# Kernel tuning notes

Hardware: AMD Instinct MI355X
Metric: run time of the kernel (lower is better)

Reference implementation:

```python
import jax, jax.numpy as jnp
import numpy as np

B, S, D, H = 1, 1024, 4096, 32
HD = D // H
HEAVY_RATIO = 0.1
RECENT_RATIO = 0.1


def _rotary_tables(seq_len, dim):
    inv_freq = 1.0 / (10000.0 ** (jnp.arange(0, dim, 2, dtype=jnp.float32) / dim))
    t = jnp.arange(seq_len, dtype=jnp.float32)
    freqs = jnp.outer(t, inv_freq)            # [S, dim/2]
    emb = jnp.concatenate([freqs, freqs], -1)  # [S, dim]
    return jnp.cos(emb), jnp.sin(emb)


def _rotate_half(x):
    x1, x2 = jnp.split(x, 2, axis=-1)
    return jnp.concatenate([-x2, x1], axis=-1)


def setup_inputs() -> dict:
    key = jax.random.key(0)
    ks = jax.random.split(key, 5)
    hidden_states = jax.random.normal(ks[0], (B, S, D), dtype=jnp.float32)
    neg = jnp.finfo(jnp.float32).min
    i = jnp.arange(S)[:, None]
    j = jnp.arange(S)[None, :]
    attention_mask = jnp.where(j <= i, 0.0, neg).astype(jnp.float32)[None, None]  # [1,1,S,S]
    std = 0.02
    Wq = jax.random.normal(ks[1], (D, D), dtype=jnp.float32) * std
    Wk = jax.random.normal(ks[2], (D, D), dtype=jnp.float32) * std
    Wv = jax.random.normal(ks[3], (D, D), dtype=jnp.float32) * std
    Wo = jax.random.normal(ks[4], (D, D), dtype=jnp.float32) * std
    return {"hidden_states": hidden_states, "attention_mask": attention_mask,
            "Wq": Wq, "Wk": Wk, "Wv": Wv, "Wo": Wo}


def _heavy_hitter_mask(attn_weights, heavy_budget):
    # attn_weights: [B,H,S,S] (already includes additive causal mask)
    b, h, s, _ = attn_weights.shape
    probs = jax.nn.softmax(attn_weights.astype(jnp.float32), axis=-1)  # [B,H,S,S]
    cols = jnp.arange(s)
    # accumulated score from the first heavy_budget rows; zero cols >= heavy_budget
    acc0 = probs[:, :, :heavy_budget, :].sum(axis=2) * (cols < heavy_budget)

    def scatter_true(idx):  # idx [k] -> [S] bool
        return jnp.zeros((s,), dtype=bool).at[idx].set(True)

    def step(acc, xs):
        prob_row, t = xs  # prob_row [B,H,S]
        _, topk_idx = jax.lax.top_k(acc, heavy_budget - 1)  # [B,H,k]
        m = jax.vmap(jax.vmap(scatter_true))(topk_idx)       # [B,H,S]
        m = m | (cols < 4) | (cols == t)
        acc = (acc + prob_row) * m
        return acc, m

    ts = jnp.arange(heavy_budget, s)
    rows = jnp.moveaxis(probs[:, :, heavy_budget:, :], 2, 0)  # [S-hb,B,H,S]
    _, masks = jax.lax.scan(step, acc0, (rows, ts))
    masks = jnp.moveaxis(masks, 0, 2)  # [B,H,S-hb,S]
    rows_i = jnp.arange(s)[:, None]
    init_block = (rows_i < heavy_budget) & (cols[None, :] < heavy_budget)  # [S,S]
    init_rows = jnp.broadcast_to(init_block[None, None, :heavy_budget, :], (b, h, heavy_budget, s))
    return jnp.concatenate([init_rows, masks], axis=2)  # [B,H,S,S] bool


def reference(hidden_states, attention_mask, Wq, Wk, Wv, Wo):
    bsz, q_len, d = hidden_states.shape
    hd = d // H
    # torch Linear: y = x @ W.T
    q = jnp.einsum('bsd,ed->bse', hidden_states, Wq).reshape(bsz, q_len, H, hd).transpose(0, 2, 1, 3)
    k = jnp.einsum('bsd,ed->bse', hidden_states, Wk).reshape(bsz, q_len, H, hd).transpose(0, 2, 1, 3)
    v = jnp.einsum('bsd,ed->bse', hidden_states, Wv).reshape(bsz, q_len, H, hd).transpose(0, 2, 1, 3)
    cos, sin = _rotary_tables(q_len, hd)  # [S,hd]
    cos = cos[None, None]; sin = sin[None, None]
    q = q * cos + _rotate_half(q) * sin
    k = k * cos + _rotate_half(k) * sin
    attn = jnp.einsum('bhqd,bhkd->bhqk', q, k) / jnp.sqrt(jnp.float32(hd))
    neg = jnp.finfo(attn.dtype).min
    attn = jnp.maximum(attn + attention_mask, neg)
    heavy_budget = int(HEAVY_RATIO * q_len)
    recent_budget = int(RECENT_RATIO * q_len)
    if heavy_budget > 0:
        mask_bottom = _heavy_hitter_mask(attn, heavy_budget)
    else:
        mask_bottom = jnp.zeros(attn.shape, dtype=bool)
    i = jnp.arange(q_len)[:, None]
    j = jnp.arange(q_len)[None, :]
    recent = j >= (i - recent_budget)        # triu(diagonal=-recent_budget)
    mask_bottom = (mask_bottom | recent) & (j <= i)  # then tril(diagonal=0)
    attn = jnp.where(mask_bottom, attn, jnp.min(attention_mask))
    attn = jax.nn.softmax(attn.astype(jnp.float32), axis=-1).astype(hidden_states.dtype)
    out = jnp.einsum('bhqk,bhkd->bhqd', attn, v)
    out = out.transpose(0, 2, 1, 3).reshape(bsz, q_len, d)
    return jnp.einsum('bse,de->bsd', out, Wo)
```

## Files before the change

kernel.cpp:

```cpp
#include <hip/hip_runtime.h>
#include <cstdint>

#define HEADS 32
#define SEQ 1024
#define HD 128
#define DMODEL 4096
#define HB 102
#define RB 102
#define KEEP 101

typedef _Float16 half8_t __attribute__((ext_vector_type(8)));
typedef _Float16 half4_t __attribute__((ext_vector_type(4)));
typedef float f32x4 __attribute__((ext_vector_type(4)));

template<bool SPLIT, int OUTMODE>
__global__ __launch_bounds__(256)
void gemm_f16(const float* __restrict__ Ag, const float* __restrict__ Bg,
              float* __restrict__ Cg, int K, int N,
              long sA, long sB, long sC, float scale)
{
    constexpr int NSP = SPLIT ? 2 : 1;
    __shared__ __align__(16) _Float16 AH[NSP][128][40];
    __shared__ __align__(16) _Float16 BH[NSP][128][40];

    const int b = blockIdx.z;
    const float* A = Ag + (long)b * sA;
    const float* Bm = Bg + (long)b * sB;
    float* C = Cg + (long)b * sC;

    const int m0 = blockIdx.y * 128, n0 = blockIdx.x * 128;
    const int tid = threadIdx.x;
    const int lane = tid & 63, wid = tid >> 6;
    const int wm = (wid & 1) * 64, wn = (wid >> 1) * 64;
    const int l16 = lane & 15, quad = lane >> 4;

    f32x4 zero4 = {0.f, 0.f, 0.f, 0.f};
    f32x4 acc[4][4];
    for (int i = 0; i < 4; ++i)
        for (int j = 0; j < 4; ++j) acc[i][j] = zero4;

    const int sr = tid >> 1;
    const int sc = (tid & 1) * 16;

    for (int k0 = 0; k0 < K; k0 += 32) {
        const float* srcA = A + (long)(m0 + sr) * K + k0 + sc;
        const float* srcB = Bm + (long)(n0 + sr) * K + k0 + sc;
#pragma unroll
        for (int i = 0; i < 4; ++i) {
            float4 v = ((const float4*)srcA)[i];
            _Float16 h0 = (_Float16)v.x, h1 = (_Float16)v.y,
                     h2 = (_Float16)v.z, h3 = (_Float16)v.w;
            *(half4_t*)&AH[0][sr][sc + 4*i] = (half4_t){h0, h1, h2, h3};
            if (SPLIT)
                *(half4_t*)&AH[NSP-1][sr][sc + 4*i] = (half4_t){
                    (_Float16)(v.x - (float)h0), (_Float16)(v.y - (float)h1),
                    (_Float16)(v.z - (float)h2), (_Float16)(v.w - (float)h3)};
            float4 w = ((const float4*)srcB)[i];
            _Float16 g0 = (_Float16)w.x, g1 = (_Float16)w.y,
                     g2 = (_Float16)w.z, g3 = (_Float16)w.w;
            *(half4_t*)&BH[0][sr][sc + 4*i] = (half4_t){g0, g1, g2, g3};
            if (SPLIT)
                *(half4_t*)&BH[NSP-1][sr][sc + 4*i] = (half4_t){
                    (_Float16)(w.x - (float)g0), (_Float16)(w.y - (float)g1),
                    (_Float16)(w.z - (float)g2), (_Float16)(w.w - (float)g3)};
        }
        __syncthreads();

        half8_t ah[4], bh[4], al[4], bl[4];
#pragma unroll
        for (int i = 0; i < 4; ++i) {
            ah[i] = *(const half8_t*)&AH[0][wm + i*16 + l16][quad * 8];
            bh[i] = *(const half8_t*)&BH[0][wn + i*16 + l16][quad * 8];
            if (SPLIT) {
                al[i] = *(const half8_t*)&AH[NSP-1][wm + i*16 + l16][quad * 8];
                bl[i] = *(const half8_t*)&BH[NSP-1][wn + i*16 + l16][quad * 8];
            }
        }
#pragma unroll
        for (int mt = 0; mt < 4; ++mt)
#pragma unroll
            for (int nt = 0; nt < 4; ++nt) {
                acc[mt][nt] = __builtin_amdgcn_mfma_f32_16x16x32_f16(ah[mt], bh[nt], acc[mt][nt], 0, 0, 0);
                if (SPLIT) {
                    acc[mt][nt] = __builtin_amdgcn_mfma_f32_16x16x32_f16(ah[mt], bl[nt], acc[mt][nt], 0, 0, 0);
                    acc[mt][nt] = __builtin_amdgcn_mfma_f32_16x16x32_f16(al[mt], bh[nt], acc[mt][nt], 0, 0, 0);
                }
            }
        __syncthreads();
    }

#pragma unroll
    for (int mt = 0; mt < 4; ++mt)
#pragma unroll
        for (int nt = 0; nt < 4; ++nt)
#pragma unroll
            for (int r = 0; r < 4; ++r) {
                int row = m0 + wm + mt*16 + quad*4 + r;
                int col = n0 + wn + nt*16 + l16;
                float v = acc[mt][nt][r] * scale;
                if (OUTMODE == 0)
                    C[(long)row * N + col] = v;
                else
                    C[(long)(col >> 7) * (SEQ * HD) + (long)row * HD + (col & 127)] = v;
            }
}

__global__ __launch_bounds__(256)
void rope_kernel(float* __restrict__ Q, float* __restrict__ Kr)
{
    int idx = blockIdx.x * 256 + threadIdx.x;
    if (idx >= HEADS * SEQ * 64) return;
    int d = idx & 63;
    int s = (idx >> 6) & (SEQ - 1);
    int h = idx >> 16;
    long base = ((long)h * SEQ + s) * HD;
    float inv = 1.0f / powf(10000.0f, (float)(2 * d) / 128.0f);
    float ang = (float)s * inv;
    float c = cosf(ang), sn = sinf(ang);
    float q1 = Q[base + d], q2 = Q[base + d + 64];
    Q[base + d]      = q1 * c - q2 * sn;
    Q[base + d + 64] = q2 * c + q1 * sn;
    float k1 = Kr[base + d], k2 = Kr[base + d + 64];
    Kr[base + d]      = k1 * c - k2 * sn;
    Kr[base + d + 64] = k2 * c + k1 * sn;
}

__global__ __launch_bounds__(64)
void stats_kernel(const float* __restrict__ S, const uint32_t* __restrict__ mb,
                  float* __restrict__ mx_o, float* __restrict__ rd_o, int phase)
{
    int row = blockIdx.x;
    int t = row & (SEQ - 1);
    const float* Sr = S + (long)row * SEQ;
    const uint32_t* mrow = mb + (long)row * 32;
    int tid = threadIdx.x;
    bool use_mask = (phase == 2) && (t >= HB);

    float lm = -3.4e38f;
    for (int j = tid; j <= t; j += 64) {
        bool ok = !use_mask || (j >= t - RB) || ((mrow[j >> 5] >> (j & 31)) & 1);
        if (ok) lm = fmaxf(lm, Sr[j]);
    }
#pragma unroll
    for (int off = 32; off; off >>= 1) lm = fmaxf(lm, __shfl_xor(lm, off));

    float ls = 0.f;
    for (int j = tid; j <= t; j += 64) {
        bool ok = !use_mask || (j >= t - RB) || ((mrow[j >> 5] >> (j & 31)) & 1);
        if (ok) ls += expf(Sr[j] - lm);
    }
#pragma unroll
    for (int off = 32; off; off >>= 1) ls += __shfl_xor(ls, off);

    if (tid == 0) { mx_o[row] = lm; rd_o[row] = 1.0f / ls; }
}

__device__ __forceinline__ uint32_t wave_umin_bcast(uint32_t v)
{
    uint32_t t;
    t = (uint32_t)__builtin_amdgcn_update_dpp((int)v, (int)v, 0x111, 0xf, 0xf, false); v = t < v ? t : v;
    t = (uint32_t)__builtin_amdgcn_update_dpp((int)v, (int)v, 0x112, 0xf, 0xf, false); v = t < v ? t : v;
    t = (uint32_t)__builtin_amdgcn_update_dpp((int)v, (int)v, 0x114, 0xf, 0xe, false); v = t < v ? t : v;
    t = (uint32_t)__builtin_amdgcn_update_dpp((int)v, (int)v, 0x118, 0xf, 0xc, false); v = t < v ? t : v;
    t = (uint32_t)__builtin_amdgcn_update_dpp((int)v, (int)v, 0x142, 0xa, 0xf, false); v = t < v ? t : v;
    t = (uint32_t)__builtin_amdgcn_update_dpp((int)v, (int)v, 0x143, 0xc, 0xf, false); v = t < v ? t : v;
    return (uint32_t)__builtin_amdgcn_readlane((int)v, 63);
}

__global__ __launch_bounds__(64)
void scan_kernel(const float* __restrict__ S, const float* __restrict__ mx1,
                 const float* __restrict__ rd1, uint32_t* __restrict__ mb)
{
    const int h = blockIdx.x, tid = threadIdx.x;
    const float* Sh = S + (long)h * SEQ * SEQ;
    const float* mx = mx1 + h * SEQ;
    const float* rd = rd1 + h * SEQ;
    __shared__ uint32_t bm[32];

    int col0 = tid, col1 = 64 + tid;
    bool al0 = true, al1 = (col1 < HB);
    float ac0 = 0.f, ac1 = 0.f;

    for (int t = 0; t < HB; ++t) {
        float m = mx[t], r = rd[t];
        if (t >= col0) ac0 += __expf(Sh[(long)t * SEQ + col0] - m) * r;
        if (al1 && t >= col1) ac1 += __expf(Sh[(long)t * SEQ + col1] - m) * r;
    }

    float x0 = Sh[(long)HB * SEQ + col0];
    float x1 = Sh[(long)HB * SEQ + col1];
    float xt = Sh[(long)HB * SEQ + HB];

    int P = HB;
    for (int t = HB; t < SEQ; ++t) {
        uint32_t k0 = al0 ? __float_as_uint(ac0) : 0xFFFFFFFFu;
        uint32_t k1 = al1 ? __float_as_uint(ac1) : 0xFFFFFFFFu;

        int nex = P - KEEP;
        for (int e = 0; e < nex; ++e) {
            uint32_t m = wave_umin_bcast(k0 < k1 ? k0 : k1);
            bool hit0 = (k0 == m), hit1 = (k1 == m);
            unsigned long long b0 = __ballot(hit0), b1 = __ballot(hit1);
            if (__popcll(b0) + __popcll(b1) > 1) {
                int c = hit0 ? col0 : -1;
                int c2 = hit1 ? col1 : -1;
                c = c > c2 ? c : c2;
#pragma unroll
                for (int off = 32; off; off >>= 1) {
                    int o = __shfl_xor(c, off);
                    c = o > c ? o : c;
                }
                hit0 = hit0 && (col0 == c);
                hit1 = hit1 && (col1 == c);
            }
            if (hit0)      { k0 = 0xFFFFFFFFu; if (col0 >= 4) al0 = false; }
            else if (hit1) { k1 = 0xFFFFFFFFu; if (col1 >= 4) al1 = false; }
        }

        bool claimed0 = false, claimed1 = false;
        unsigned long long d0 = __ballot(!al0);
        if (d0) {
            claimed0 = (tid == __ffsll(d0) - 1);
        } else {
            unsigned long long d1 = __ballot(!al1);
            claimed1 = (tid == __ffsll(d1) - 1);
        }
        if (claimed0) { col0 = t; ac0 = 0.f; al0 = true; }
        if (claimed1) { col1 = t; ac1 = 0.f; al1 = true; }
        P = __popcll(__ballot(al0)) + __popcll(__ballot(al1));

        float nx0 = 0.f, nx1 = 0.f, nxt = 0.f;
        if (t + 1 < SEQ) {
            const float* Sn = Sh + (long)(t + 1) * SEQ;
            nx0 = Sn[col0]; nx1 = Sn[col1]; nxt = Sn[t + 1];
        }

        float sm = mx[t], sr = rd[t];
        if (al0) ac0 += __expf((claimed0 ? xt : x0) - sm) * sr;
        if (al1) ac1 += __expf((claimed1 ? xt : x1) - sm) * sr;
        x0 = nx0; x1 = nx1; xt = nxt;

        if (tid < 32) bm[tid] = 0;
        if (al0) atomicOr(&bm[col0 >> 5], 1u << (col0 & 31));
        if (al1) atomicOr(&bm[col1 >> 5], 1u << (col1 & 31));
        if (tid < 32) mb[((long)h * SEQ + t) * 32 + tid] = bm[tid];
    }
}

__global__ __launch_bounds__(256)
void pv_kernel(const float* __restrict__ S, const float* __restrict__ V,
               const uint32_t* __restrict__ mb, const float* __restrict__ mx2,
               const float* __restrict__ rd2, float* __restrict__ ctx)
{
    const int rb = blockIdx.x, h = blockIdx.y;
    const int tid = threadIdx.x, lane = tid & 63, wid = tid >> 6;
    const int wm = (wid & 1) * 32, wn = (wid >> 1) * 64;
    const int l16 = lane & 15, quad = lane >> 4;
    __shared__ __align__(16) _Float16 PT[64][72];
    __shared__ __align__(16) _Float16 VT[128][72];

    const int m0 = rb * 64;
    f32x4 zero4 = {0.f, 0.f, 0.f, 0.f};
    f32x4 acc[2][4];
    for (int i = 0; i < 2; ++i)
        for (int j = 0; j < 4; ++j) acc[i][j] = zero4;

    const float* Sh = S + ((long)h * SEQ + m0) * SEQ;
    const float* Vh = V + (long)h * SEQ * HD;

    const int pr = tid >> 2, pc = (tid & 3) * 16;
    const int trow = m0 + pr;
    const float pmx = mx2[h * SEQ + trow], prd = rd2[h * SEQ + trow];
    const uint32_t* mrow = mb + ((long)h * SEQ + trow) * 32;
    const bool use_mask = (trow >= HB);

    for (int jt = 0; jt <= rb; ++jt) {
        int j0 = jt * 64;
#pragma unroll
        for (int i = 0; i < 4; ++i) {
            float4 v = *(const float4*)(Sh + (long)pr * SEQ + j0 + pc + i * 4);
#pragma unroll
            for (int u = 0; u < 4; ++u) {
                int j = j0 + pc + i * 4 + u;
                float s = (u == 0) ? v.x : (u == 1) ? v.y : (u == 2) ? v.z : v.w;
                bool ok = (j <= trow) &&
                          (!use_mask || j >= trow - RB || ((mrow[j >> 5] >> (j & 31)) & 1));
                float p = ok ? expf(s - pmx) * prd : 0.f;
                PT[pr][pc + i * 4 + u] = (_Float16)p;
            }
        }
#pragma unroll
        for (int i = 0; i < 8; ++i) {
            int flat = i * 256 + tid;
            int j = flat >> 5, c4 = (flat & 31) * 4;
            float4 v = *(const float4*)(Vh + (long)(j0 + j) * HD + c4);
            VT[c4 + 0][j] = (_Float16)v.x;
            VT[c4 + 1][j] = (_Float16)v.y;
            VT[c4 + 2][j] = (_Float16)v.z;
            VT[c4 + 3][j] = (_Float16)v.w;
        }
        __syncthreads();
#pragma unroll
        for (int ks = 0; ks < 2; ++ks) {
            half8_t a[2], bf[4];
#pragma unroll
            for (int i = 0; i < 2; ++i)
                a[i] = *(const half8_t*)&PT[wm + i * 16 + l16][ks * 32 + quad * 8];
#pragma unroll
            for (int i = 0; i < 4; ++i)
                bf[i] = *(const half8_t*)&VT[wn + i * 16 + l16][ks * 32 + quad * 8];
#pragma unroll
            for (int mt = 0; mt < 2; ++mt)
#pragma unroll
                for (int nt = 0; nt < 4; ++nt)
                    acc[mt][nt] = __builtin_amdgcn_mfma_f32_16x16x32_f16(a[mt], bf[nt], acc[mt][nt], 0, 0, 0);
        }
        __syncthreads();
    }
#pragma unroll
    for (int mt = 0; mt < 2; ++mt)
#pragma unroll
        for (int nt = 0; nt < 4; ++nt)
#pragma unroll
            for (int r = 0; r < 4; ++r) {
                int s_ = m0 + wm + mt * 16 + quad * 4 + r;
                int hd = wn + nt * 16 + l16;
                ctx[(long)s_ * DMODEL + h * HD + hd] = acc[mt][nt][r];
            }
}

extern "C" void kernel_launch(void* const* d_in, const int* in_sizes, int n_in,
                              void* d_out, int out_size, void* d_ws, size_t ws_size,
                              hipStream_t stream)
{
    const float* hs = (const float*)d_in[0];
    const float* Wq = (const float*)d_in[2];
    const float* Wk = (const float*)d_in[3];
    const float* Wv = (const float*)d_in[4];
    const float* Wo = (const float*)d_in[5];
    float* out = (float*)d_out;

    char* w = (char*)d_ws;
    float* Qr  = (float*)w;  w += (long)HEADS * SEQ * HD * 4;
    float* Kr  = (float*)w;  w += (long)HEADS * SEQ * HD * 4;
    float* V   = (float*)w;  w += (long)HEADS * SEQ * HD * 4;
    float* ctx = (float*)w;  w += (long)SEQ * DMODEL * 4;
    float* mx1 = (float*)w;  w += (long)HEADS * SEQ * 4;
    float* rd1 = (float*)w;  w += (long)HEADS * SEQ * 4;
    float* mx2 = (float*)w;  w += (long)HEADS * SEQ * 4;
    float* rd2 = (float*)w;  w += (long)HEADS * SEQ * 4;
    uint32_t* mb = (uint32_t*)w; w += (long)HEADS * SEQ * 32 * 4;
    float* S   = (float*)w;  w += (long)HEADS * SEQ * SEQ * 4;

    const float inv_sqrt_hd = 0.088388347648318447f;

    dim3 gproj(DMODEL / 128, SEQ / 128, 1);
    gemm_f16<true, 1><<<gproj, 256, 0, stream>>>(hs, Wq, Qr, DMODEL, DMODEL, 0, 0, 0, 1.f);
    gemm_f16<true, 1><<<gproj, 256, 0, stream>>>(hs, Wk, Kr, DMODEL, DMODEL, 0, 0, 0, 1.f);
    gemm_f16<false, 1><<<gproj, 256, 0, stream>>>(hs, Wv, V, DMODEL, DMODEL, 0, 0, 0, 1.f);

    rope_kernel<<<(HEADS * SEQ * 64) / 256, 256, 0, stream>>>(Qr, Kr);

    dim3 gsc(SEQ / 128, SEQ / 128, HEADS);
    gemm_f16<true, 0><<<gsc, 256, 0, stream>>>(Qr, Kr, S, HD, SEQ,
        (long)SEQ * HD, (long)SEQ * HD, (long)SEQ * SEQ, inv_sqrt_hd);

    stats_kernel<<<HEADS * SEQ, 64, 0, stream>>>(S, mb, mx1, rd1, 1);
    scan_kernel<<<HEADS, 64, 0, stream>>>(S, mx1, rd1, mb);
    stats_kernel<<<HEADS * SEQ, 64, 0, stream>>>(S, mb, mx2, rd2, 2);
    pv_kernel<<<dim3(SEQ / 64, HEADS), 256, 0, stream>>>(S, V, mb, mx2, rd2, ctx);

    gemm_f16<false, 0><<<gproj, 256, 0, stream>>>(ctx, Wo, out, DMODEL, DMODEL, 0, 0, 0, 1.f);
}
```

Baseline: 1.930 ms.

## Prefetch scan rows three steps ahead and keep bitmask in registers

The sequential heavy-hitter scan kernel now prefetches the score row, the max and the reciprocal values three iterations ahead through a register rotation, so global-load latency is hidden behind the eviction loop. A small window of four values near the diagonal handles columns that were just claimed. The per-step shared-memory bitmask rebuild with atomics and a barrier-free store is replaced by a per-lane register word that is updated incrementally on eviction and claim. This adds register pressure and more complex index logic, and the incremental bitmask must stay in exact agreement with the active-column set.

Measured after the change: 1.936 ms. No clear change (+0.3%).

```diff
diff --git a/kernel.cpp b/kernel.cpp
--- a/kernel.cpp
+++ b/kernel.cpp
@@ -175,7 +175,6 @@
     const float* Sh = S + (long)h * SEQ * SEQ;
     const float* mx = mx1 + h * SEQ;
     const float* rd = rd1 + h * SEQ;
-    __shared__ uint32_t bm[32];
 
     int col0 = tid, col1 = 64 + tid;
     bool al0 = true, al1 = (col1 < HB);
@@ -187,20 +186,41 @@
         if (al1 && t >= col1) ac1 += __expf(Sh[(long)t * SEQ + col1] - m) * r;
     }
 
-    float x0 = Sh[(long)HB * SEQ + col0];
-    float x1 = Sh[(long)HB * SEQ + col1];
-    float xt = Sh[(long)HB * SEQ + HB];
+    uint32_t bmw = (tid < 3) ? 0xFFFFFFFFu : (tid == 3 ? 0x3Fu : 0u);
+
+    float x0a, x0b, x0c, x1a, x1b, x1c;
+    f32x4 bqa, bqb, bqc;
+    float mqa, mqb, mqc, rqa, rqb, rqc;
+    {
+        const float* r0 = Sh + (long)(HB + 0) * SEQ;
+        const float* r1 = Sh + (long)(HB + 1) * SEQ;
+        const float* r2 = Sh + (long)(HB + 2) * SEQ;
+        x0a = r0[col0]; x1a = r0[col1];
+        x0b = r1[col0]; x1b = r1[col1];
+        x0c = r2[col0]; x1c = r2[col1];
+        bqa = (f32x4){r0[HB - 3], r0[HB - 2], r0[HB - 1], r0[HB + 0]};
+        bqb = (f32x4){r1[HB - 2], r1[HB - 1], r1[HB + 0], r1[HB + 1]};
+        bqc = (f32x4){r2[HB - 1], r2[HB + 0], r2[HB + 1], r2[HB + 2]};
+        mqa = mx[HB]; mqb = mx[HB + 1]; mqc = mx[HB + 2];
+        rqa = rd[HB]; rqb = rd[HB + 1]; rqc = rd[HB + 2];
+    }
 
     int P = HB;
     for (int t = HB; t < SEQ; ++t) {
+        int u = t + 3; if (u > SEQ - 1) u = SEQ - 1;
+        const float* Sn = Sh + (long)u * SEQ;
+        float nx0 = Sn[col0], nx1 = Sn[col1];
+        f32x4 nbq = (f32x4){Sn[u - 3], Sn[u - 2], Sn[u - 1], Sn[u]};
+        float nmq = mx[u], nrq = rd[u];
+
         uint32_t k0 = al0 ? __float_as_uint(ac0) : 0xFFFFFFFFu;
         uint32_t k1 = al1 ? __float_as_uint(ac1) : 0xFFFFFFFFu;
-
         int nex = P - KEEP;
         for (int e = 0; e < nex; ++e) {
-            uint32_t m = wave_umin_bcast(k0 < k1 ? k0 : k1);
-            bool hit0 = (k0 == m), hit1 = (k1 == m);
+            uint32_t mn = wave_umin_bcast(k0 < k1 ? k0 : k1);
+            bool hit0 = (k0 == mn), hit1 = (k1 == mn);
             unsigned long long b0 = __ballot(hit0), b1 = __ballot(hit1);
+            int vc;
             if (__popcll(b0) + __popcll(b1) > 1) {
                 int c = hit0 ? col0 : -1;
                 int c2 = hit1 ? col1 : -1;
@@ -211,39 +231,44 @@
                     c = o > c ? o : c;
                 }
                 hit0 = hit0 && (col0 == c);
-                hit1 = hit1 && (col1 == c);
+                hit1 = hit1 && (col1 == c) && !hit0;
+                vc = c;
+            } else {
+                int ln = (int)(__ffsll(b0 | b1) - 1);
+                int vsel = hit0 ? col0 : col1;
+                vc = __shfl(vsel, ln);
             }
             if (hit0)      { k0 = 0xFFFFFFFFu; if (col0 >= 4) al0 = false; }
             else if (hit1) { k1 = 0xFFFFFFFFu; if (col1 >= 4) al1 = false; }
+            if (vc >= 4 && tid == (vc >> 5)) bmw &= ~(1u << (vc & 31));
         }
 
         bool claimed0 = false, claimed1 = false;
         unsigned long long d0 = __ballot(!al0);
-        if (d0) {
-            claimed0 = (tid == __ffsll(d0) - 1);
-        } else {
-            unsigned long long d1 = __ballot(!al1);
-            claimed1 = (tid == __ffsll(d1) - 1);
-        }
+        unsigned long long d1 = __ballot(!al1);
+        if (d0)      claimed0 = (tid == __ffsll(d0) - 1);
+        else if (d1) claimed1 = (tid == __ffsll(d1) - 1);
         if (claimed0) { col0 = t; ac0 = 0.f; al0 = true; }
         if (claimed1) { col1 = t; ac1 = 0.f; al1 = true; }
+        if ((d0 | d1) && tid == (t >> 5)) bmw |= 1u << (t & 31);
         P = __popcll(__ballot(al0)) + __popcll(__ballot(al1));
 
-        float nx0 = 0.f, nx1 = 0.f, nxt = 0.f;
-        if (t + 1 < SEQ) {
-            const float* Sn = Sh + (long)(t + 1) * SEQ;
-            nx0 = Sn[col0]; nx1 = Sn[col1]; nxt = Sn[t + 1];
-        }
-
-        float sm = mx[t], sr = rd[t];
-        if (al0) ac0 += __expf((claimed0 ? xt : x0) - sm) * sr;
-        if (al1) ac1 += __expf((claimed1 ? xt : x1) - sm) * sr;
-        x0 = nx0; x1 = nx1; xt = nxt;
-
-        if (tid < 32) bm[tid] = 0;
-        if (al0) atomicOr(&bm[col0 >> 5], 1u << (col0 & 31));
-        if (al1) atomicOr(&bm[col1 >> 5], 1u << (col1 & 31));
-        if (tid < 32) mb[((long)h * SEQ + t) * 32 + tid] = bm[tid];
+        float v0 = x0a;
+        int j0 = col0 - (t - 3);
+        if (j0 >= 0) v0 = (j0 == 3) ? bqa[3] : (j0 == 2) ? bqa[2] : (j0 == 1) ? bqa[1] : bqa[0];
+        float v1 = x1a;
+        int j1 = col1 - (t - 3);
+        if (j1 >= 0) v1 = (j1 == 3) ? bqa[3] : (j1 == 2) ? bqa[2] : (j1 == 1) ? bqa[1] : bqa[0];
+        if (al0) ac0 += __expf(v0 - mqa) * rqa;
+        if (al1) ac1 += __expf(v1 - mqa) * rqa;
+
+        if (tid < 32) mb[((long)h * SEQ + t) * 32 + tid] = bmw;
+
+        x0a = x0b; x0b = x0c; x0c = nx0;
+        x1a = x1b; x1b = x1c; x1c = nx1;
+        bqa = bqb; bqb = bqc; bqc = nbq;
+        mqa = mqb; mqb = mqc; mqc = nmq;
+        rqa = rqb; rqb = rqc; rqc = nrq;
     }
 }
 
```
